# Optimization experiments

Hardware: AMD Instinct MI355X
Metric: run time of the kernel (lower is better)

## Reference

```python
import jax, jax.numpy as jnp
import numpy as np

B, T, D, H = 128, 512, 1024, 1024


def setup_inputs() -> dict:
    key = jax.random.key(0)
    k_x, k_wx, k_wh = jax.random.split(key, 3)
    # PyTorch Linear init scale ~ U(-1/sqrt(fan_in), 1/sqrt(fan_in)); normal*0.03 is fine for a numeric baseline
    x = jax.random.normal(k_x, (B, T, D), dtype=jnp.float32)
    adjacency = jnp.zeros((T, T), dtype=jnp.float32)  # accepted by the torch module but unused
    Wx = jax.random.normal(k_wx, (4, D, H), dtype=jnp.float32) * (1.0 / np.sqrt(D))
    Wh = jax.random.normal(k_wh, (4, H, H), dtype=jnp.float32) * (1.0 / np.sqrt(H))
    b = jnp.zeros((4, H), dtype=jnp.float32)
    return {"x": x, "adjacency": adjacency, "Wx": Wx, "Wh": Wh, "b": b}


def _tree_lstm(x, Wx, Wh, b):
    # x: [B, T, D]; gate order: i, f, o, u
    xt = jnp.transpose(x, (1, 0, 2))  # [T, B, D]
    # precompute all input projections in one big batched GEMM: [T, 4, B, H]
    x_gates = jnp.einsum('tbd,gdh->tgbh', xt, Wx)
    h0 = jnp.zeros((x.shape[0], Wh.shape[1]), dtype=x.dtype)
    c0 = jnp.zeros_like(h0)

    def step(carry, xg_t):
        h, c = carry
        gates = xg_t + jnp.einsum('bh,ghk->gbk', h, Wh) + b[:, None, :]  # [4, B, H]
        i_t = jax.nn.sigmoid(gates[0])
        f_t = jax.nn.sigmoid(gates[1])
        o_t = jax.nn.sigmoid(gates[2])
        u_t = jnp.tanh(gates[3])
        c_new = f_t * c + i_t * u_t
        h_new = o_t * jnp.tanh(c_new)  # dropout is identity at inference
        return (h_new, c_new), None

    (h, _), _ = jax.lax.scan(step, (h0, c0), x_gates)
    return h  # [B, H]


def reference(x, adjacency, Wx, Wh, b):
    del adjacency  # unused in the original forward
    return _tree_lstm(x, Wx, Wh, b)
```

## Files before the change

kernel.cpp:

```cpp
#include <hip/hip_runtime.h>
#include <hip/hip_bf16.h>

typedef __attribute__((ext_vector_type(8))) short bf16x8;
typedef __attribute__((ext_vector_type(4))) float f32x4;

#define NBLK 256
#define NTHR 512

__device__ __forceinline__ unsigned short f2bf(float f) {
  unsigned int u = __float_as_uint(f);
  unsigned int r = (u + 0x7FFFu + ((u >> 16) & 1u)) >> 16;
  return (unsigned short)r;
}

__device__ __forceinline__ bf16x8 ldg_b128_coh(const unsigned short* p) {
  bf16x8 r;
  asm volatile("global_load_dwordx4 %0, %1, off sc0 sc1"
               : "=v"(r) : "v"(p) : "memory");
  return r;
}
__device__ __forceinline__ void stg_b16_coh(unsigned short* p, unsigned v) {
  asm volatile("global_store_short %0, %1, off sc0 sc1"
               :: "v"(p), "v"(v) : "memory");
}

__global__ __launch_bounds__(256) void pack_w(const float* __restrict__ Wx,
                                              const float* __restrict__ Wh,
                                              unsigned short* __restrict__ Wp) {
  int idx = blockIdx.x * 256 + threadIdx.x;
  int k  = idx & 2047;
  int c  = (idx >> 11) & 31;
  int jb = idx >> 16;
  int g  = c & 3;
  int j  = jb * 8 + (c >> 2);
  float v = (k < 1024) ? Wh[((size_t)(g * 1024 + k)) * 1024 + j]
                       : Wx[((size_t)(g * 1024 + (k - 1024))) * 1024 + j];
  Wp[idx] = f2bf(v);
}

__global__ __launch_bounds__(256) void pack_x(const float* __restrict__ x,
                                              unsigned short* __restrict__ xpk) {
  size_t idx = (size_t)blockIdx.x * 256 + threadIdx.x;
  int lane = (int)(idx & 63);
  int wr   = (int)((idx >> 6) & 3);
  int s    = (int)((idx >> 8) & 15);
  int wn   = (int)((idx >> 12) & 1);
  int rb   = (int)((idx >> 13) & 1);
  int t    = (int)(idx >> 14);
  int a15 = lane & 15, hi = lane >> 4;
  int row = rb * 64 + wr * 16 + a15;
  int k   = (2 * s + wn) * 32 + hi * 8;
  const float* src = x + ((size_t)row * 512 + t) * 1024 + k;
  float4 f0 = *(const float4*)src;
  float4 f1 = *(const float4*)(src + 4);
  float fl[8] = {f0.x, f0.y, f0.z, f0.w, f1.x, f1.y, f1.z, f1.w};
  union { bf16x8 v; unsigned short us[8]; } u;
  #pragma unroll
  for (int e = 0; e < 8; ++e) u.us[e] = f2bf(fl[e]);
  *(bf16x8*)(xpk + idx * 8) = u.v;
}

__global__ __launch_bounds__(512, 2) void lstm_persist(
    const float* __restrict__ x,
    const unsigned short* __restrict__ xpk,
    const unsigned short* __restrict__ Wp,
    const float* __restrict__ bias,
    unsigned short* __restrict__ h0,
    unsigned short* __restrict__ h1,
    float* __restrict__ out,
    unsigned* __restrict__ bar)
{
  __shared__ unsigned short Wlds[32][2052];
  __shared__ float gt[2][64][33];

  const int tid = threadIdx.x;
  const int bx  = blockIdx.x;
  const int xcd = bx & 7;
  const int rb  = xcd >> 2;
  const int jb  = (bx >> 3) * 4 + (xcd & 3);
  const int row0 = rb * 64;

  #pragma unroll
  for (int rep = 0; rep < 16; ++rep) {
    int ch = rep * 512 + tid;
    int c  = ch >> 8;
    int k8 = (ch & 255) * 8;
    *(bf16x8*)&Wlds[c][k8] = *(const bf16x8*)(Wp + ((size_t)(jb * 32 + c)) * 2048 + k8);
  }

  const int lane = tid & 63;
  const int w    = tid >> 6;
  const int wr   = w >> 1;
  const int wn   = w & 1;
  const int a15  = lane & 15;
  const int hi   = lane >> 4;

  const int um  = tid >> 3;
  const int uj  = tid & 7;
  const int ujg = jb * 8 + uj;
  const float bi = bias[ujg], bf_ = bias[1024 + ujg];
  const float bo = bias[2048 + ujg], bu = bias[3072 + ujg];
  float creg = 0.f;

  const int rowg = row0 + wr * 16 + a15;
  const float* xrow = x + (size_t)rowg * 512 * 1024;
  const size_t xpk_lane = ((size_t)wr * 64 + lane) * 8;

  __syncthreads();

  unsigned short* hb[2] = {h0, h1};
  bf16x8 xreg[16];

  if (xpk) {
    const unsigned short* xs = xpk + ((((size_t)0 * 2 + rb) * 2 + wn) * 16) * 2048 + xpk_lane;
    #pragma unroll
    for (int s = 0; s < 16; ++s) {
      const unsigned short* p = xs + s * 2048;
      asm volatile("global_load_dwordx4 %0, %1, off" : "=v"(xreg[s]) : "v"(p) : "memory");
    }
  } else {
    const float* xt = xrow + hi * 8;
    #pragma unroll
    for (int s = 0; s < 16; ++s) {
      const float* xp = xt + (2 * s + wn) * 32;
      float4 f0 = *(const float4*)xp;
      float4 f1 = *(const float4*)(xp + 4);
      float fl[8] = {f0.x, f0.y, f0.z, f0.w, f1.x, f1.y, f1.z, f1.w};
      union { bf16x8 v; unsigned short us[8]; } u;
      #pragma unroll
      for (int e = 0; e < 8; ++e) u.us[e] = f2bf(fl[e]);
      xreg[s] = u.v;
    }
  }

  for (int t = 0; t < 512; ++t) {
    const unsigned short* hc = hb[t & 1];
    unsigned short* hn = hb[(t + 1) & 1];

    f32x4 acc0 = {}, acc1 = {};

    bf16x8 hreg[16];
    const unsigned short* hbase = hc + (size_t)rowg * 1024 + hi * 8;
    #pragma unroll
    for (int s = 0; s < 16; ++s)
      hreg[s] = ldg_b128_coh(hbase + (2 * s + wn) * 32);

    asm volatile("s_waitcnt vmcnt(16)" ::: "memory");
    __builtin_amdgcn_sched_barrier(0);
    #pragma unroll
    for (int s = 0; s < 16; ++s) {
      const int kk = 1024 + (2 * s + wn) * 32 + hi * 8;
      bf16x8 b0 = *(const bf16x8*)&Wlds[a15][kk];
      bf16x8 b1 = *(const bf16x8*)&Wlds[16 + a15][kk];
      acc0 = __builtin_amdgcn_mfma_f32_16x16x32_bf16(xreg[s], b0, acc0, 0, 0, 0);
      acc1 = __builtin_amdgcn_mfma_f32_16x16x32_bf16(xreg[s], b1, acc1, 0, 0, 0);
    }

    asm volatile("s_waitcnt vmcnt(0)" ::: "memory");
    __builtin_amdgcn_sched_barrier(0);
    #pragma unroll
    for (int s = 0; s < 16; ++s) {
      const int kk = (2 * s + wn) * 32 + hi * 8;
      bf16x8 b0 = *(const bf16x8*)&Wlds[a15][kk];
      bf16x8 b1 = *(const bf16x8*)&Wlds[16 + a15][kk];
      acc0 = __builtin_amdgcn_mfma_f32_16x16x32_bf16(hreg[s], b0, acc0, 0, 0, 0);
      acc1 = __builtin_amdgcn_mfma_f32_16x16x32_bf16(hreg[s], b1, acc1, 0, 0, 0);
    }

    #pragma unroll
    for (int r = 0; r < 4; ++r) {
      gt[wn][wr * 16 + hi * 4 + r][a15]      = acc0[r];
      gt[wn][wr * 16 + hi * 4 + r][16 + a15] = acc1[r];
    }
    __syncthreads();

    float vi = gt[0][um][uj * 4 + 0] + gt[1][um][uj * 4 + 0] + bi;
    float vf = gt[0][um][uj * 4 + 1] + gt[1][um][uj * 4 + 1] + bf_;
    float vo = gt[0][um][uj * 4 + 2] + gt[1][um][uj * 4 + 2] + bo;
    float vu = gt[0][um][uj * 4 + 3] + gt[1][um][uj * 4 + 3] + bu;
    float iv = 1.f / (1.f + expf(-vi));
    float fv = 1.f / (1.f + expf(-vf));
    float ov = 1.f / (1.f + expf(-vo));
    float uv = tanhf(vu);
    creg = fv * creg + iv * uv;
    float hv = ov * tanhf(creg);
    stg_b16_coh(hn + (size_t)(row0 + um) * 1024 + ujg, (unsigned)f2bf(hv));
    if (t == 511) {
      out[(size_t)(row0 + um) * 1024 + ujg] = hv;
      break;
    }

    if (xpk) {
      const unsigned short* xs = xpk + ((((size_t)(t + 1) * 2 + rb) * 2 + wn) * 16) * 2048 + xpk_lane;
      #pragma unroll
      for (int s = 0; s < 16; ++s) {
        const unsigned short* p = xs + s * 2048;
        asm volatile("global_load_dwordx4 %0, %1, off" : "=v"(xreg[s]) : "v"(p) : "memory");
      }
    } else {
      const float* xt = xrow + (size_t)(t + 1) * 1024 + hi * 8;
      #pragma unroll
      for (int s = 0; s < 16; ++s) {
        const float* xp = xt + (2 * s + wn) * 32;
        float4 f0 = *(const float4*)xp;
        float4 f1 = *(const float4*)(xp + 4);
        float fl[8] = {f0.x, f0.y, f0.z, f0.w, f1.x, f1.y, f1.z, f1.w};
        union { bf16x8 v; unsigned short us[8]; } u;
        #pragma unroll
        for (int e = 0; e < 8; ++e) u.us[e] = f2bf(fl[e]);
        xreg[s] = u.v;
      }
    }

    asm volatile("s_waitcnt vmcnt(16)" ::: "memory");
    __builtin_amdgcn_s_barrier();
    if (tid == 0) {
      unsigned g = (unsigned)(bx & 7);
      unsigned prev = __hip_atomic_fetch_add(&bar[g * 32], 1u, __ATOMIC_RELAXED,
                                             __HIP_MEMORY_SCOPE_AGENT);
      if ((prev & 31u) == 31u) {
        unsigned rp = __hip_atomic_fetch_add(&bar[256], 1u, __ATOMIC_RELAXED,
                                             __HIP_MEMORY_SCOPE_AGENT);
        if ((rp & 7u) == 7u)
          __hip_atomic_fetch_add(&bar[320], 1u, __ATOMIC_RELAXED,
                                 __HIP_MEMORY_SCOPE_AGENT);
      }
      while (__hip_atomic_load(&bar[320], __ATOMIC_RELAXED,
                               __HIP_MEMORY_SCOPE_AGENT) <= (unsigned)t)
        __builtin_amdgcn_s_sleep(4);
    }
    __builtin_amdgcn_s_barrier();
  }
}

extern "C" void kernel_launch(void* const* d_in, const int* in_sizes, int n_in,
                              void* d_out, int out_size, void* d_ws, size_t ws_size,
                              hipStream_t stream) {
  const float* x    = (const float*)d_in[0];
  const float* Wx   = (const float*)d_in[2];
  const float* Wh   = (const float*)d_in[3];
  const float* bias = (const float*)d_in[4];
  float* out = (float*)d_out;

  char* ws = (char*)d_ws;
  unsigned short* Wp = (unsigned short*)ws;
  unsigned short* h0 = (unsigned short*)(ws + 16777216);
  unsigned short* h1 = h0 + 128 * 1024;
  unsigned* bar = (unsigned*)(ws + 16777216 + 2 * 262144);
  const size_t XPK_OFF = 33554432;
  const size_t XPK_SZ  = 134217728;
  unsigned short* xpk = (ws_size >= XPK_OFF + XPK_SZ)
                        ? (unsigned short*)(ws + XPK_OFF) : nullptr;

  pack_w<<<32768, 256, 0, stream>>>(Wx, Wh, Wp);
  if (xpk) pack_x<<<32768, 256, 0, stream>>>(x, xpk);
  hipMemsetAsync(h0, 0, 128 * 1024 * sizeof(unsigned short), stream);
  hipMemsetAsync(bar, 0, 2048, stream);

  (void)in_sizes; (void)n_in;
  lstm_persist<<<NBLK, NTHR, 0, stream>>>(x, xpk, Wp, bias, h0, h1, out, bar);
}
```

Measured before the change: 4.618 ms.

## Replace global atomic barrier with per-row-block flag polling and split h-wait

Replaces the hierarchical atomic-counter grid barrier with per-block step flags. Each block stores its step after writing h, and each block's wavefronts poll only the flags of the blocks sharing its row block, via a vectorized coherent load. It also splits the recurrent MFMA loop so the first half of the h tiles is consumed once 8 loads land, and moves the x prefetch after the flag store. This cuts synchronization latency on the sequential critical path. It relies on every wave polling with correct memory visibility, and the additional waitcnt(0) before the flag store may serialize some loads.

```diff
diff --git a/kernel.cpp b/kernel.cpp
--- a/kernel.cpp
+++ b/kernel.cpp
@@ -3,6 +3,7 @@
 
 typedef __attribute__((ext_vector_type(8))) short bf16x8;
 typedef __attribute__((ext_vector_type(4))) float f32x4;
+typedef __attribute__((ext_vector_type(2))) unsigned uint32x2;
 
 #define NBLK 256
 #define NTHR 512
@@ -105,6 +106,7 @@
   const int rowg = row0 + wr * 16 + a15;
   const float* xrow = x + (size_t)rowg * 512 * 1024;
   const size_t xpk_lane = ((size_t)wr * 64 + lane) * 8;
+  const unsigned* fpoll = bar + rb * 128 + (lane << 1);
 
   __syncthreads();
 
@@ -112,12 +114,12 @@
   bf16x8 xreg[16];
 
   if (xpk) {
-    const unsigned short* xs = xpk + ((((size_t)0 * 2 + rb) * 2 + wn) * 16) * 2048 + xpk_lane;
-    #pragma unroll
-    for (int s = 0; s < 16; ++s) {
-      const unsigned short* p = xs + s * 2048;
-      asm volatile("global_load_dwordx4 %0, %1, off" : "=v"(xreg[s]) : "v"(p) : "memory");
-    }
+    const unsigned short* xs = xpk + (((size_t)0 * 2 + rb) * 2 + wn) * 16 * 2048 + xpk_lane;
+    #pragma unroll
+    for (int s = 0; s < 16; ++s)
+      asm volatile("global_load_dwordx4 %0, %1, off" : "=v"(xreg[s]) : "v"(xs + s * 2048) : "memory");
+    asm volatile("s_waitcnt vmcnt(0)" ::: "memory");
+    __builtin_amdgcn_sched_barrier(0);
   } else {
     const float* xt = xrow + hi * 8;
     #pragma unroll
@@ -137,16 +139,14 @@
     const unsigned short* hc = hb[t & 1];
     unsigned short* hn = hb[(t + 1) & 1];
 
-    f32x4 acc0 = {}, acc1 = {};
-
     bf16x8 hreg[16];
     const unsigned short* hbase = hc + (size_t)rowg * 1024 + hi * 8;
     #pragma unroll
     for (int s = 0; s < 16; ++s)
       hreg[s] = ldg_b128_coh(hbase + (2 * s + wn) * 32);
-
-    asm volatile("s_waitcnt vmcnt(16)" ::: "memory");
-    __builtin_amdgcn_sched_barrier(0);
+    __builtin_amdgcn_sched_barrier(0);
+
+    f32x4 acc0 = {}, acc1 = {};
     #pragma unroll
     for (int s = 0; s < 16; ++s) {
       const int kk = 1024 + (2 * s + wn) * 32 + hi * 8;
@@ -156,10 +156,20 @@
       acc1 = __builtin_amdgcn_mfma_f32_16x16x32_bf16(xreg[s], b1, acc1, 0, 0, 0);
     }
 
+    asm volatile("s_waitcnt vmcnt(8)" ::: "memory");
+    __builtin_amdgcn_sched_barrier(0);
+    #pragma unroll
+    for (int s = 0; s < 8; ++s) {
+      const int kk = (2 * s + wn) * 32 + hi * 8;
+      bf16x8 b0 = *(const bf16x8*)&Wlds[a15][kk];
+      bf16x8 b1 = *(const bf16x8*)&Wlds[16 + a15][kk];
+      acc0 = __builtin_amdgcn_mfma_f32_16x16x32_bf16(hreg[s], b0, acc0, 0, 0, 0);
+      acc1 = __builtin_amdgcn_mfma_f32_16x16x32_bf16(hreg[s], b1, acc1, 0, 0, 0);
+    }
     asm volatile("s_waitcnt vmcnt(0)" ::: "memory");
     __builtin_amdgcn_sched_barrier(0);
     #pragma unroll
-    for (int s = 0; s < 16; ++s) {
+    for (int s = 8; s < 16; ++s) {
       const int kk = (2 * s + wn) * 32 + hi * 8;
       bf16x8 b0 = *(const bf16x8*)&Wlds[a15][kk];
       bf16x8 b1 = *(const bf16x8*)&Wlds[16 + a15][kk];
@@ -190,13 +200,20 @@
       break;
     }
 
+    asm volatile("s_waitcnt vmcnt(0)" ::: "memory");
+    __builtin_amdgcn_s_barrier();
+    if (tid == 0) {
+      const unsigned* p = bar + rb * 128 + jb;
+      unsigned val = (unsigned)(t + 1);
+      asm volatile("global_store_dword %0, %1, off sc0 sc1"
+                   :: "v"(p), "v"(val) : "memory");
+    }
+
     if (xpk) {
-      const unsigned short* xs = xpk + ((((size_t)(t + 1) * 2 + rb) * 2 + wn) * 16) * 2048 + xpk_lane;
+      const unsigned short* xs = xpk + (((size_t)(t + 1) * 2 + rb) * 2 + wn) * 16 * 2048 + xpk_lane;
       #pragma unroll
-      for (int s = 0; s < 16; ++s) {
-        const unsigned short* p = xs + s * 2048;
-        asm volatile("global_load_dwordx4 %0, %1, off" : "=v"(xreg[s]) : "v"(p) : "memory");
-      }
+      for (int s = 0; s < 16; ++s)
+        asm volatile("global_load_dwordx4 %0, %1, off" : "=v"(xreg[s]) : "v"(xs + s * 2048) : "memory");
     } else {
       const float* xt = xrow + (size_t)(t + 1) * 1024 + hi * 8;
       #pragma unroll
@@ -212,24 +229,15 @@
       }
     }
 
-    asm volatile("s_waitcnt vmcnt(16)" ::: "memory");
-    __builtin_amdgcn_s_barrier();
-    if (tid == 0) {
-      unsigned g = (unsigned)(bx & 7);
-      unsigned prev = __hip_atomic_fetch_add(&bar[g * 32], 1u, __ATOMIC_RELAXED,
-                                             __HIP_MEMORY_SCOPE_AGENT);
-      if ((prev & 31u) == 31u) {
-        unsigned rp = __hip_atomic_fetch_add(&bar[256], 1u, __ATOMIC_RELAXED,
-                                             __HIP_MEMORY_SCOPE_AGENT);
-        if ((rp & 7u) == 7u)
-          __hip_atomic_fetch_add(&bar[320], 1u, __ATOMIC_RELAXED,
-                                 __HIP_MEMORY_SCOPE_AGENT);
-      }
-      while (__hip_atomic_load(&bar[320], __ATOMIC_RELAXED,
-                               __HIP_MEMORY_SCOPE_AGENT) <= (unsigned)t)
-        __builtin_amdgcn_s_sleep(4);
-    }
-    __builtin_amdgcn_s_barrier();
+    for (;;) {
+      uint32x2 v;
+      asm volatile("global_load_dwordx2 %0, %1, off sc0 sc1"
+                   : "=v"(v) : "v"(fpoll) : "memory");
+      asm volatile("s_waitcnt vmcnt(0)" ::: "memory");
+      if (__all(v.x > (unsigned)t && v.y > (unsigned)t)) break;
+      __builtin_amdgcn_s_sleep(1);
+    }
+    __builtin_amdgcn_sched_barrier(0);
   }
 }
 
@@ -255,7 +263,7 @@
   pack_w<<<32768, 256, 0, stream>>>(Wx, Wh, Wp);
   if (xpk) pack_x<<<32768, 256, 0, stream>>>(x, xpk);
   hipMemsetAsync(h0, 0, 128 * 1024 * sizeof(unsigned short), stream);
-  hipMemsetAsync(bar, 0, 2048, stream);
+  hipMemsetAsync(bar, 0, 4096, stream);
 
   (void)in_sizes; (void)n_in;
   lstm_persist<<<NBLK, NTHR, 0, stream>>>(x, xpk, Wp, bias, h0, h1, out, bar);
```

Result: faster. 3.797 ms (-17.8%).
